# Kernel tuning notes

Measured on AMD Instinct MI355X. Metric: run time of the kernel, lower is better.

The kernel has to match this reference:

```python
import jax, jax.numpy as jnp
import numpy as np

N_NODES = 20000
N_EDGES = 320000
HID = 128
IN_NODE = 128
IN_EDGE = 128
OUT = 64
N_LAYERS = 5 - 2  # 3 layers
EPS = 1e-5


def _lin_init(k, din, dout):
    return jax.random.normal(k, (din, dout), jnp.float32) * (1.0 / np.sqrt(din))


def setup_inputs() -> dict:
    key = jax.random.key(0)
    ks = jax.random.split(key, 12)
    h = jax.random.normal(ks[0], (N_NODES, IN_NODE), jnp.float32)
    edge_index = jax.random.randint(ks[1], (2, N_EDGES), 0, N_NODES, jnp.int64)
    edge_attr = jax.random.normal(ks[2], (N_EDGES, IN_EDGE), jnp.float32)
    node_emb_W = _lin_init(ks[3], IN_NODE, HID)
    node_emb_b = jnp.zeros((HID,), jnp.float32)
    edge_emb_W = _lin_init(ks[4], IN_EDGE, HID)
    edge_emb_b = jnp.zeros((HID,), jnp.float32)
    # 5 linears (A,B,C,D,E) per layer, stacked: [L, 5, HID, HID]
    layers_W = jax.random.normal(ks[5], (N_LAYERS, 5, HID, HID), jnp.float32) * (1.0 / np.sqrt(HID))
    layers_b = jax.random.normal(ks[6], (N_LAYERS, 5, HID), jnp.float32) * 0.01
    # bn params: index 0 = node BN, index 1 = edge BN
    bn_gamma = jnp.ones((N_LAYERS, 2, HID), jnp.float32)
    bn_beta = jnp.zeros((N_LAYERS, 2, HID), jnp.float32)
    cls_W1 = _lin_init(ks[7], HID, HID)
    cls_b1 = jnp.zeros((HID,), jnp.float32)
    cls_W2 = _lin_init(ks[8], HID, OUT)
    cls_b2 = jnp.zeros((OUT,), jnp.float32)
    return dict(h=h, edge_index=edge_index, edge_attr=edge_attr,
                node_emb_W=node_emb_W, node_emb_b=node_emb_b,
                edge_emb_W=edge_emb_W, edge_emb_b=edge_emb_b,
                layers_W=layers_W, layers_b=layers_b,
                bn_gamma=bn_gamma, bn_beta=bn_beta,
                cls_W1=cls_W1, cls_b1=cls_b1, cls_W2=cls_W2, cls_b2=cls_b2)


def _bn(x, g, b):
    # BatchNorm1d in train mode: batch mean / biased variance per feature
    mu = jnp.mean(x, axis=0)
    var = jnp.mean((x - mu) ** 2, axis=0)
    return g * (x - mu) * jax.lax.rsqrt(var + EPS) + b


def _forward(h, edge_attr, edge_index, node_emb_W, node_emb_b, edge_emb_W,
             edge_emb_b, layers_W, layers_b, bn_gamma, bn_beta,
             cls_W1, cls_b1, cls_W2, cls_b2):
    n = h.shape[0]
    src, dst = edge_index[0], edge_index[1]
    h = h @ node_emb_W + node_emb_b            # [N, HID]
    e = edge_attr @ edge_emb_W + edge_emb_b    # [E, HID]
    for l in range(layers_W.shape[0]):
        W, b = layers_W[l], layers_b[l]
        Ah = h @ W[0] + b[0]
        Bh = h @ W[1] + b[1]
        Ce = e @ W[2] + b[2]
        Dh = h @ W[3] + b[3]
        Eh = h @ W[4] + b[4]
        e_hat = Ce + Dh[dst] + Eh[src]         # [E, HID]
        sigma = jax.nn.sigmoid(e_hat)
        # edge update: BN -> ReLU -> (dropout p=0) -> residual
        e = e + jax.nn.relu(_bn(e_hat, bn_gamma[l, 1], bn_beta[l, 1]))
        # node update: scatter-add of sigma * Bh[src] onto dst
        agg = jax.ops.segment_sum(sigma * Bh[src], dst, num_segments=n)
        h = h + jax.nn.relu(_bn(Ah + agg, bn_gamma[l, 0], bn_beta[l, 0]))
    out = jnp.mean(h, axis=0, keepdims=True)   # [1, HID]
    out = jax.nn.relu(out @ cls_W1 + cls_b1) @ cls_W2 + cls_b2
    return out


def reference(h, edge_index, edge_attr, node_emb_W, node_emb_b, edge_emb_W,
              edge_emb_b, layers_W, layers_b, bn_gamma, bn_beta,
              cls_W1, cls_b1, cls_W2, cls_b2):
    return _forward(h, edge_attr, edge_index, node_emb_W, node_emb_b,
                    edge_emb_W, edge_emb_b, layers_W, layers_b,
                    bn_gamma, bn_beta, cls_W1, cls_b1, cls_W2, cls_b2)
```

## Files before the change

kernel.cpp:

```cpp
#include <hip/hip_runtime.h>
#include <math.h>

#define NN 20000
#define NE 320000
#define NL 3
#define EPSV 1e-5f
#define MAXD 128
#define ASZ 2560

#define S_ESC  0
#define S_ESH  128
#define S_NSC  256
#define S_NSH  384
#define S_TOTAL 512

typedef __attribute__((ext_vector_type(8))) short bf16x8;
typedef __attribute__((ext_vector_type(4))) float f32x4;

__device__ __forceinline__ float sigf(float x) { return 1.0f / (1.0f + expf(-x)); }
__device__ __forceinline__ float b2f(unsigned short s) { return __uint_as_float((unsigned)s << 16); }
__device__ __forceinline__ unsigned short f2b(float a)
{
  unsigned u = __float_as_uint(a);
  return (unsigned short)((u + 0x7FFFu + ((u >> 16) & 1u)) >> 16);
}

__device__ __forceinline__ void bsplit(float a, unsigned short& h, unsigned short& l)
{
  unsigned u = __float_as_uint(a);
  unsigned rh = (u + 0x7FFFu + ((u >> 16) & 1u)) >> 16;
  h = (unsigned short)rh;
  float hf = __uint_as_float(rh << 16);
  float d = a - hf;
  unsigned v = __float_as_uint(d);
  l = (unsigned short)((v + 0x7FFFu + ((v >> 16) & 1u)) >> 16);
}

__global__ __launch_bounds__(256) void prep_w(const float* __restrict__ src,
                                              unsigned short* __restrict__ dh,
                                              unsigned short* __restrict__ dl, int nmat)
{
  int idx = blockIdx.x * 256 + threadIdx.x;
  if (idx >= nmat * 16384) return;
  int m = idx >> 14, r = idx & 16383, k = r >> 7, c = r & 127;
  unsigned short h, l;
  bsplit(src[idx], h, l);
  long o = ((long)m << 14) + c * 128 + k;
  dh[o] = h; dl[o] = l;
}

__device__ __forceinline__ void loadWfrags(const unsigned short* __restrict__ Wh_g,
                                           const unsigned short* __restrict__ Wl_g,
                                           int k0, int w, int r16, int g8,
                                           bf16x8& h0, bf16x8& h1, bf16x8& l0, bf16x8& l1)
{
  long o0 = (long)(w * 32 + r16) * 128 + k0 + g8 * 8;
  long o1 = o0 + 16 * 128;
  h0 = *(const bf16x8*)(Wh_g + o0);
  h1 = *(const bf16x8*)(Wh_g + o1);
  l0 = *(const bf16x8*)(Wl_g + o0);
  l1 = *(const bf16x8*)(Wl_g + o1);
}
__device__ __forceinline__ void writeA_pair(const float4& a, int row, int c4,
                                            unsigned short* Ah, unsigned short* Al)
{
  unsigned short h0, l0, h1, l1, h2, l2, h3, l3;
  bsplit(a.x, h0, l0); bsplit(a.y, h1, l1); bsplit(a.z, h2, l2); bsplit(a.w, h3, l3);
  *(uint2*)(Ah + row * 40 + c4 * 4) =
      make_uint2((unsigned)h0 | ((unsigned)h1 << 16), (unsigned)h2 | ((unsigned)h3 << 16));
  *(uint2*)(Al + row * 40 + c4 * 4) =
      make_uint2((unsigned)l0 | ((unsigned)l1 << 16), (unsigned)l2 | ((unsigned)l3 << 16));
}
__device__ __forceinline__ void writeA_bf(const float4& a, int row, int c4, unsigned short* Ah)
{
  *(uint2*)(Ah + row * 40 + c4 * 4) = make_uint2(
      (unsigned)f2b(a.x) | ((unsigned)f2b(a.y) << 16),
      (unsigned)f2b(a.z) | ((unsigned)f2b(a.w) << 16));
}

__device__ __forceinline__ void mfma_frags3r(int r16, int g8, f32x4 acc[4][2],
    const unsigned short* Ah, const unsigned short* Al,
    bf16x8 wh0, bf16x8 wh1, bf16x8 wl0, bf16x8 wl1)
{
  bf16x8 ah[4], al[4];
  #pragma unroll
  for (int rg = 0; rg < 4; ++rg) {
    ah[rg] = *(const bf16x8*)(Ah + (rg * 16 + r16) * 40 + g8 * 8);
    al[rg] = *(const bf16x8*)(Al + (rg * 16 + r16) * 40 + g8 * 8);
  }
  #pragma unroll
  for (int rg = 0; rg < 4; ++rg) {
    acc[rg][0] = __builtin_amdgcn_mfma_f32_16x16x32_bf16(ah[rg], wh0, acc[rg][0], 0, 0, 0);
    acc[rg][0] = __builtin_amdgcn_mfma_f32_16x16x32_bf16(ah[rg], wl0, acc[rg][0], 0, 0, 0);
    acc[rg][0] = __builtin_amdgcn_mfma_f32_16x16x32_bf16(al[rg], wh0, acc[rg][0], 0, 0, 0);
    acc[rg][1] = __builtin_amdgcn_mfma_f32_16x16x32_bf16(ah[rg], wh1, acc[rg][1], 0, 0, 0);
    acc[rg][1] = __builtin_amdgcn_mfma_f32_16x16x32_bf16(ah[rg], wl1, acc[rg][1], 0, 0, 0);
    acc[rg][1] = __builtin_amdgcn_mfma_f32_16x16x32_bf16(al[rg], wh1, acc[rg][1], 0, 0, 0);
  }
}

__device__ __forceinline__ void mfma_frags2r(int r16, int g8, f32x4 acc[4][2],
    const unsigned short* Ah,
    bf16x8 wh0, bf16x8 wh1, bf16x8 wl0, bf16x8 wl1)
{
  bf16x8 ah[4];
  #pragma unroll
  for (int rg = 0; rg < 4; ++rg)
    ah[rg] = *(const bf16x8*)(Ah + (rg * 16 + r16) * 40 + g8 * 8);
  #pragma unroll
  for (int rg = 0; rg < 4; ++rg) {
    acc[rg][0] = __builtin_amdgcn_mfma_f32_16x16x32_bf16(ah[rg], wh0, acc[rg][0], 0, 0, 0);
    acc[rg][0] = __builtin_amdgcn_mfma_f32_16x16x32_bf16(ah[rg], wl0, acc[rg][0], 0, 0, 0);
    acc[rg][1] = __builtin_amdgcn_mfma_f32_16x16x32_bf16(ah[rg], wh1, acc[rg][1], 0, 0, 0);
    acc[rg][1] = __builtin_amdgcn_mfma_f32_16x16x32_bf16(ah[rg], wl1, acc[rg][1], 0, 0, 0);
  }
}

#define ACC_INIT                          \
  _Pragma("unroll")                       \
  for (int rg = 0; rg < 4; ++rg)          \
    _Pragma("unroll")                     \
    for (int cg = 0; cg < 2; ++cg)        \
      acc[rg][cg] = (f32x4){0.f, 0.f, 0.f, 0.f};

__device__ __forceinline__ void mfma_core_f32(
    const float* __restrict__ A, long base, int M,
    const unsigned short* __restrict__ Wh_g, const unsigned short* __restrict__ Wl_g,
    int tid, f32x4 acc[4][2], unsigned short* Ah, unsigned short* Al)
{
  int lane = tid & 63, w = tid >> 6, r16 = lane & 15, g8 = lane >> 4;
  int r0 = tid >> 3, c4 = tid & 7;
  long g0 = base + r0, g1 = g0 + 32;
  bool v0 = g0 < M, v1 = g1 < M;
  ACC_INIT
  float4 a[4][2];
  #pragma unroll
  for (int ks = 0; ks < 4; ++ks) {
    a[ks][0] = v0 ? *(const float4*)(A + g0 * 128 + ks * 32 + c4 * 4) : make_float4(0.f, 0.f, 0.f, 0.f);
    a[ks][1] = v1 ? *(const float4*)(A + g1 * 128 + ks * 32 + c4 * 4) : make_float4(0.f, 0.f, 0.f, 0.f);
  }
  bf16x8 wc0, wc1, wc2, wc3, wn0, wn1, wn2, wn3;
  loadWfrags(Wh_g, Wl_g, 0, w, r16, g8, wc0, wc1, wc2, wc3);
  writeA_pair(a[0][0], r0, c4, Ah, Al);
  writeA_pair(a[0][1], r0 + 32, c4, Ah, Al);
  #pragma unroll
  for (int ks = 0; ks < 4; ++ks) {
    __syncthreads();
    int cb = ks & 1, nb = cb ^ 1;
    if (ks < 3) loadWfrags(Wh_g, Wl_g, 32 * (ks + 1), w, r16, g8, wn0, wn1, wn2, wn3);
    mfma_frags3r(r16, g8, acc, Ah + cb * ASZ, Al + cb * ASZ, wc0, wc1, wc2, wc3);
    if (ks < 3) {
      writeA_pair(a[ks + 1][0], r0, c4, Ah + nb * ASZ, Al + nb * ASZ);
      writeA_pair(a[ks + 1][1], r0 + 32, c4, Ah + nb * ASZ, Al + nb * ASZ);
      wc0 = wn0; wc1 = wn1; wc2 = wn2; wc3 = wn3;
    }
  }
}

__device__ __forceinline__ void mfma_core_bf16i(
    const float* __restrict__ A, const int* ridx,
    const unsigned short* __restrict__ Wh_g, const unsigned short* __restrict__ Wl_g,
    int tid, f32x4 acc[4][2], unsigned short* Ah)
{
  int lane = tid & 63, w = tid >> 6, r16 = lane & 15, g8 = lane >> 4;
  int r0 = tid >> 3, c4 = tid & 7;
  long g0 = ridx[r0], g1 = ridx[r0 + 32];
  ACC_INIT
  float4 a[4][2];
  #pragma unroll
  for (int ks = 0; ks < 4; ++ks) {
    a[ks][0] = *(const float4*)(A + g0 * 128 + ks * 32 + c4 * 4);
    a[ks][1] = *(const float4*)(A + g1 * 128 + ks * 32 + c4 * 4);
  }
  bf16x8 wc0, wc1, wc2, wc3, wn0, wn1, wn2, wn3;
  loadWfrags(Wh_g, Wl_g, 0, w, r16, g8, wc0, wc1, wc2, wc3);
  writeA_bf(a[0][0], r0, c4, Ah);
  writeA_bf(a[0][1], r0 + 32, c4, Ah);
  #pragma unroll
  for (int ks = 0; ks < 4; ++ks) {
    __syncthreads();
    int cb = ks & 1, nb = cb ^ 1;
    if (ks < 3) loadWfrags(Wh_g, Wl_g, 32 * (ks + 1), w, r16, g8, wn0, wn1, wn2, wn3);
    mfma_frags2r(r16, g8, acc, Ah + cb * ASZ, wc0, wc1, wc2, wc3);
    if (ks < 3) {
      writeA_bf(a[ks + 1][0], r0, c4, Ah + nb * ASZ);
      writeA_bf(a[ks + 1][1], r0 + 32, c4, Ah + nb * ASZ);
      wc0 = wn0; wc1 = wn1; wc2 = wn2; wc3 = wn3;
    }
  }
}

__device__ __forceinline__ void mfma_core_bf16(
    const unsigned short* __restrict__ Abf, long base,
    const unsigned short* __restrict__ Wh_g, const unsigned short* __restrict__ Wl_g,
    int tid, f32x4 acc[4][2], unsigned short* Ah)
{
  int lane = tid & 63, w = tid >> 6, r16 = lane & 15, g8 = lane >> 4;
  int row = tid >> 2, q = tid & 3;
  ACC_INIT
  long gof = (base + row) * 128 + q * 8;
  uint4 av[4];
  #pragma unroll
  for (int ks = 0; ks < 4; ++ks) av[ks] = *(const uint4*)(Abf + gof + ks * 32);
  bf16x8 wc0, wc1, wc2, wc3, wn0, wn1, wn2, wn3;
  loadWfrags(Wh_g, Wl_g, 0, w, r16, g8, wc0, wc1, wc2, wc3);
  *(uint4*)(Ah + row * 40 + q * 8) = av[0];
  #pragma unroll
  for (int ks = 0; ks < 4; ++ks) {
    __syncthreads();
    int cb = ks & 1, nb = cb ^ 1;
    if (ks < 3) loadWfrags(Wh_g, Wl_g, 32 * (ks + 1), w, r16, g8, wn0, wn1, wn2, wn3);
    mfma_frags2r(r16, g8, acc, Ah + cb * ASZ, wc0, wc1, wc2, wc3);
    if (ks < 3) {
      *(uint4*)(Ah + nb * ASZ + row * 40 + q * 8) = av[ks + 1];
      wc0 = wn0; wc1 = wn1; wc2 = wn2; wc3 = wn3;
    }
  }
}

template<bool WB>
__device__ __forceinline__ void mfma_core_upd(
    unsigned short* __restrict__ Ebf,
    const unsigned short* __restrict__ EHAT, long base,
    const unsigned short* __restrict__ Wh_g, const unsigned short* __restrict__ Wl_g,
    const float* s_sc, const float* s_sh,
    int tid, f32x4 acc[4][2], unsigned short* Ah)
{
  int lane = tid & 63, w = tid >> 6, r16 = lane & 15, g8 = lane >> 4;
  int row = tid >> 2, q = tid & 3;
  ACC_INIT
  long grow = (base + row) * 128;
  uint4 ev[4], hv[4];
  #pragma unroll
  for (int ks = 0; ks < 4; ++ks) {
    ev[ks] = *(const uint4*)(Ebf + grow + ks * 32 + q * 8);
    hv[ks] = *(const uint4*)(EHAT + grow + ks * 32 + q * 8);
  }
  bf16x8 wc0, wc1, wc2, wc3, wn0, wn1, wn2, wn3;
  loadWfrags(Wh_g, Wl_g, 0, w, r16, g8, wc0, wc1, wc2, wc3);

  #pragma unroll
  for (int ks = 0; ks < 4; ++ks) {
    int cb = ks & 1;
    int cbase = ks * 32 + q * 8;
    {
      uint4 evk = ev[ks], hvk = hv[ks];
      unsigned es[8] = {evk.x & 0xFFFFu, evk.x >> 16, evk.y & 0xFFFFu, evk.y >> 16,
                        evk.z & 0xFFFFu, evk.z >> 16, evk.w & 0xFFFFu, evk.w >> 16};
      unsigned hs[8] = {hvk.x & 0xFFFFu, hvk.x >> 16, hvk.y & 0xFFFFu, hvk.y >> 16,
                        hvk.z & 0xFFFFu, hvk.z >> 16, hvk.w & 0xFFFFu, hvk.w >> 16};
      unsigned short nv[8];
      #pragma unroll
      for (int i = 0; i < 8; ++i) {
        float v = b2f((unsigned short)es[i]) +
                  fmaxf(fmaf(s_sc[cbase + i], b2f((unsigned short)hs[i]), s_sh[cbase + i]), 0.f);
        nv[i] = f2b(v);
      }
      uint4 nq = make_uint4((unsigned)nv[0] | ((unsigned)nv[1] << 16),
                            (unsigned)nv[2] | ((unsigned)nv[3] << 16),
                            (unsigned)nv[4] | ((unsigned)nv[5] << 16),
                            (unsigned)nv[6] | ((unsigned)nv[7] << 16));
      *(uint4*)(Ah + cb * ASZ + row * 40 + q * 8) = nq;
      if (WB) *(uint4*)(Ebf + grow + cbase) = nq;
    }
    __syncthreads();
    if (ks < 3) loadWfrags(Wh_g, Wl_g, 32 * (ks + 1), w, r16, g8, wn0, wn1, wn2, wn3);
    mfma_frags2r(r16, g8, acc, Ah + cb * ASZ, wc0, wc1, wc2, wc3);
    if (ks < 3) { wc0 = wn0; wc1 = wn1; wc2 = wn2; wc3 = wn3; }
    if (ks < 2) __syncthreads();
  }
}

__device__ __forceinline__ void edge_epilogue(
    f32x4 acc[4][2], const float* __restrict__ bias,
    const int* __restrict__ srcp, const int* __restrict__ dstp,
    const float* __restrict__ Dh, const float* __restrict__ Eh,
    unsigned short* __restrict__ ehat, float* __restrict__ epart, int do_stats,
    long base, int tid)
{
  int lane = tid & 63, w = tid >> 6;
  int r16 = lane & 15, g8 = lane >> 4;
  int colA = w * 32 + r16, colB = colA + 16;
  float bA = bias[colA], bB = bias[colB];
  float s0 = 0.f, s1 = 0.f, q0 = 0.f, q1 = 0.f;
  #pragma unroll
  for (int rg = 0; rg < 4; ++rg)
    #pragma unroll
    for (int j = 0; j < 4; ++j) {
      long erow = base + rg * 16 + g8 * 4 + j;
      int si = srcp[erow], di = dstp[erow];
      const float* dhp = Dh + (long)di * 128;
      const float* ehp = Eh + (long)si * 128;
      float xA = acc[rg][0][j] + bA + dhp[colA] + ehp[colA];
      float xB = acc[rg][1][j] + bB + dhp[colB] + ehp[colB];
      ehat[erow * 128 + colA] = f2b(xA);
      ehat[erow * 128 + colB] = f2b(xB);
      s0 += xA; q0 += xA * xA; s1 += xB; q1 += xB * xB;
    }
  if (do_stats) {
    s0 += __shfl_xor(s0, 16); s0 += __shfl_xor(s0, 32);
    q0 += __shfl_xor(q0, 16); q0 += __shfl_xor(q0, 32);
    s1 += __shfl_xor(s1, 16); s1 += __shfl_xor(s1, 32);
    q1 += __shfl_xor(q1, 16); q1 += __shfl_xor(q1, 32);
    if (g8 == 0) {
      float* bp = epart + (long)blockIdx.x * 256;
      bp[colA] = s0;       bp[128 + colA] = q0;
      bp[colB] = s1;       bp[128 + colB] = q1;
    }
  }
}

__global__ __launch_bounds__(256) void gemm128(
    const float* __restrict__ A, const unsigned short* __restrict__ Wh_g,
    const unsigned short* __restrict__ Wl_g, const float* __restrict__ bias,
    float* __restrict__ C, int M)
{
  __shared__ unsigned short Ah[2 * ASZ], Al[2 * ASZ];
  int tid = threadIdx.x, lane = tid & 63, w = tid >> 6;
  int r16 = lane & 15, g8 = lane >> 4;
  long base = (long)blockIdx.x * 64;
  f32x4 acc[4][2];
  mfma_core_f32(A, base, M, Wh_g, Wl_g, tid, acc, Ah, Al);
  #pragma unroll
  for (int cg = 0; cg < 2; ++cg) {
    int col = w * 32 + cg * 16 + r16;
    float b = bias[col];
    #pragma unroll
    for (int rg = 0; rg < 4; ++rg)
      #pragma unroll
      for (int j = 0; j < 4; ++j) {
        long row = base + rg * 16 + g8 * 4 + j;
        if (row < M) C[row * 128 + col] = acc[rg][cg][j] + b;
      }
  }
}

__global__ __launch_bounds__(256) void gemm128s(
    const float* __restrict__ A, const int* __restrict__ rows,
    const unsigned short* __restrict__ Wh_g, const unsigned short* __restrict__ Wl_g,
    const float* __restrict__ bias,
    unsigned short* __restrict__ Cbf)
{
  __shared__ unsigned short Ah[2 * ASZ];
  __shared__ int ridx[64];
  int tid = threadIdx.x, lane = tid & 63, w = tid >> 6;
  int r16 = lane & 15, g8 = lane >> 4;
  long base = (long)blockIdx.x * 64;
  if (tid < 64) ridx[tid] = rows[base + tid];
  __syncthreads();
  f32x4 acc[4][2];
  mfma_core_bf16i(A, ridx, Wh_g, Wl_g, tid, acc, Ah);
  #pragma unroll
  for (int cg = 0; cg < 2; ++cg) {
    int col = w * 32 + cg * 16 + r16;
    float b = bias[col];
    #pragma unroll
    for (int rg = 0; rg < 4; ++rg)
      #pragma unroll
      for (int j = 0; j < 4; ++j) {
        long row = base + rg * 16 + g8 * 4 + j;
        Cbf[row * 128 + col] = f2b(acc[rg][cg][j] + b);
      }
  }
}

__global__ __launch_bounds__(256) void gemm128_x4(
    const float* __restrict__ A, const unsigned short* __restrict__ Wh_l,
    const unsigned short* __restrict__ Wl_l, const float* __restrict__ bl,
    float* __restrict__ o0, float* __restrict__ o1, float* __restrict__ o2,
    float* __restrict__ o3, int M)
{
  __shared__ unsigned short Ah[2 * ASZ], Al[2 * ASZ];
  int y = blockIdx.y;
  int widx = (y < 2) ? y : y + 1;
  const unsigned short* Wh_g = Wh_l + ((long)widx << 14);
  const unsigned short* Wl_g = Wl_l + ((long)widx << 14);
  const float* bias = bl + (long)widx * 128;
  float* C = (y == 0) ? o0 : (y == 1) ? o1 : (y == 2) ? o2 : o3;
  int tid = threadIdx.x, lane = tid & 63, w = tid >> 6;
  int r16 = lane & 15, g8 = lane >> 4;
  long base = (long)blockIdx.x * 64;
  f32x4 acc[4][2];
  mfma_core_f32(A, base, M, Wh_g, Wl_g, tid, acc, Ah, Al);
  #pragma unroll
  for (int cg = 0; cg < 2; ++cg) {
    int col = w * 32 + cg * 16 + r16;
    float b = bias[col];
    #pragma unroll
    for (int rg = 0; rg < 4; ++rg)
      #pragma unroll
      for (int j = 0; j < 4; ++j) {
        long row = base + rg * 16 + g8 * 4 + j;
        if (row < M) C[row * 128 + col] = acc[rg][cg][j] + b;
      }
  }
}

__global__ __launch_bounds__(256) void edge_fused0(
    const unsigned short* __restrict__ ebf,
    const unsigned short* __restrict__ Wh_g, const unsigned short* __restrict__ Wl_g,
    const float* __restrict__ bias, const int* __restrict__ srcp, const int* __restrict__ dstp,
    const float* __restrict__ Dh, const float* __restrict__ Eh,
    unsigned short* __restrict__ ehat, float* __restrict__ epart, int do_stats)
{
  __shared__ unsigned short Ah[2 * ASZ];
  int tid = threadIdx.x;
  long base = (long)blockIdx.x * 64;
  f32x4 acc[4][2];
  mfma_core_bf16(ebf, base, Wh_g, Wl_g, tid, acc, Ah);
  edge_epilogue(acc, bias, srcp, dstp, Dh, Eh, ehat, epart, do_stats, base, tid);
}

template<bool WB>
__global__ __launch_bounds__(256) void edge_fusedU(
    unsigned short* __restrict__ ebf,
    unsigned short* __restrict__ ehat,
    const float* __restrict__ scale, const float* __restrict__ shift,
    const unsigned short* __restrict__ Wh_g, const unsigned short* __restrict__ Wl_g,
    const float* __restrict__ bias, const int* __restrict__ srcp, const int* __restrict__ dstp,
    const float* __restrict__ Dh, const float* __restrict__ Eh,
    float* __restrict__ epart, int do_stats)
{
  __shared__ unsigned short Ah[2 * ASZ];
  __shared__ float s_sc[128], s_sh[128];
  int tid = threadIdx.x;
  if (tid < 128) { s_sc[tid] = scale[tid]; s_sh[tid] = shift[tid]; }
  __syncthreads();
  long base = (long)blockIdx.x * 64;
  f32x4 acc[4][2];
  mfma_core_upd<WB>(ebf, ehat, base, Wh_g, Wl_g, s_sc, s_sh, tid, acc, Ah);
  edge_epilogue(acc, bias, srcp, dstp, Dh, Eh, ehat, epart, do_stats, base, tid);
}

__global__ __launch_bounds__(256) void reduce_part(const float* __restrict__ in,
                                                   float* __restrict__ outp, int groups)
{
  int t = threadIdx.x;
  long base = (long)blockIdx.x * groups * 256;
  float acc = 0.f;
  for (int i = 0; i < groups; ++i) acc += in[base + i * 256 + t];
  outp[(long)blockIdx.x * 256 + t] = acc;
}

__global__ void finalize_bn_p(const float* __restrict__ part, int np, float invn,
                              const float* __restrict__ gamma, const float* __restrict__ beta,
                              float* __restrict__ scale, float* __restrict__ shift)
{
  int c = threadIdx.x;
  float s = 0.f, q = 0.f;
  for (int p = 0; p < np; ++p) {
    s += part[(long)p * 256 + c];
    q += part[(long)p * 256 + 128 + c];
  }
  float mu = s * invn;
  float var = q * invn - mu * mu;
  float sc = gamma[c] * rsqrtf(var + EPSV);
  scale[c] = sc;
  shift[c] = beta[c] - sc * mu;
}

__global__ __launch_bounds__(256) void hist_dst(const int* __restrict__ dst, int* __restrict__ deg)
{
  int e = blockIdx.x * 256 + threadIdx.x;
  if (e < NE) atomicAdd(&deg[dst[e]], 1);
}

__global__ __launch_bounds__(1024) void scan_deg(const int* __restrict__ deg,
                                                 int* __restrict__ rowstart, int* __restrict__ cursor)
{
  __shared__ int wsum[16];
  __shared__ int carry;
  int tid = threadIdx.x, lane = tid & 63, wid = tid >> 6;
  if (tid == 0) carry = 0;
  __syncthreads();
  for (int base = 0; base < NN; base += 1024) {
    int i = base + tid;
    int v = (i < NN) ? deg[i] : 0;
    int x = v;
    #pragma unroll
    for (int off = 1; off < 64; off <<= 1) {
      int y = __shfl_up(x, off, 64);
      if (lane >= off) x += y;
    }
    if (lane == 63) wsum[wid] = x;
    __syncthreads();
    int wpref = 0;
    for (int j = 0; j < wid; ++j) wpref += wsum[j];
    int excl = carry + wpref + x - v;
    if (i < NN) { rowstart[i] = excl; cursor[i] = excl; }
    __syncthreads();
    if (tid == 1023) carry = excl + v;
    __syncthreads();
  }
  if (tid == 0) rowstart[NN] = NE;
}

__global__ __launch_bounds__(256) void fill_csr(const int* __restrict__ dst,
                                                int* __restrict__ cursor, int* __restrict__ elist)
{
  int e = blockIdx.x * 256 + threadIdx.x;
  if (e < NE) {
    int p = atomicAdd(&cursor[dst[e]], 1);
    elist[p] = e;
  }
}

__global__ __launch_bounds__(128) void seg_sort(const int* __restrict__ rowstart,
                                                int* __restrict__ elist)
{
  __shared__ int buf[MAXD];
  __shared__ int srt[MAXD];
  int n = blockIdx.x;
  int s = rowstart[n], t = rowstart[n + 1];
  int deg = t - s;
  if (deg > MAXD) deg = MAXD;
  int tid = threadIdx.x;
  if (tid < deg) buf[tid] = elist[s + tid];
  __syncthreads();
  if (tid < deg) {
    int v = buf[tid], r = 0;
    for (int j = 0; j < deg; ++j) r += (buf[j] < v);
    srt[r] = v;
  }
  __syncthreads();
  if (tid < deg) elist[s + tid] = srt[tid];
}

__global__ __launch_bounds__(256) void perm_edges(const int* __restrict__ elist,
                                                  const int* __restrict__ src,
                                                  const int* __restrict__ dst,
                                                  int* __restrict__ srcp, int* __restrict__ dstp)
{
  int s = blockIdx.x * 256 + threadIdx.x;
  if (s < NE) {
    int e = elist[s];
    srcp[s] = src[e];
    dstp[s] = dst[e];
  }
}

__global__ __launch_bounds__(128) void gather_node(
    const unsigned short* __restrict__ ehat, const float* __restrict__ Bh,
    const int* __restrict__ srcp, const int* __restrict__ rowstart, float* __restrict__ x)
{
  __shared__ int ssrc[MAXD];
  int n = blockIdx.x;
  int s = rowstart[n], t = rowstart[n + 1];
  int deg = t - s;
  int nload = deg < MAXD ? deg : MAXD;
  int tid = threadIdx.x;
  if (tid < nload) ssrc[tid] = srcp[s + tid];
  __syncthreads();
  float acc = 0.f;
  for (int k = 0; k < nload; ++k)
    acc += sigf(b2f(ehat[(long)(s + k) * 128 + tid])) * Bh[(long)ssrc[k] * 128 + tid];
  for (int k = MAXD; k < deg; ++k)
    acc += sigf(b2f(ehat[(long)(s + k) * 128 + tid])) * Bh[(long)srcp[s + k] * 128 + tid];
  x[(long)n * 128 + tid] += acc;
}

__global__ __launch_bounds__(256) void stats128p(const float* __restrict__ x, float* __restrict__ part)
{
  __shared__ float red[8][32][8];
  int tid = threadIdx.x, tx = tid & 31, ty = tid >> 5;
  long rbase = (long)blockIdx.x * 80;
  float a0 = 0, a1 = 0, a2 = 0, a3 = 0, c0 = 0, c1 = 0, c2 = 0, c3 = 0;
  #pragma unroll
  for (int i = 0; i < 10; ++i) {
    long row = rbase + i * 8 + ty;
    float4 v = *(const float4*)(x + row * 128 + tx * 4);
    a0 += v.x; a1 += v.y; a2 += v.z; a3 += v.w;
    c0 += v.x * v.x; c1 += v.y * v.y; c2 += v.z * v.z; c3 += v.w * v.w;
  }
  red[ty][tx][0] = a0; red[ty][tx][1] = a1; red[ty][tx][2] = a2; red[ty][tx][3] = a3;
  red[ty][tx][4] = c0; red[ty][tx][5] = c1; red[ty][tx][6] = c2; red[ty][tx][7] = c3;
  __syncthreads();
  if (ty == 0) {
    float b0 = 0, b1 = 0, b2 = 0, b3 = 0, d0 = 0, d1 = 0, d2 = 0, d3 = 0;
    #pragma unroll
    for (int t = 0; t < 8; ++t) {
      b0 += red[t][tx][0]; b1 += red[t][tx][1]; b2 += red[t][tx][2]; b3 += red[t][tx][3];
      d0 += red[t][tx][4]; d1 += red[t][tx][5]; d2 += red[t][tx][6]; d3 += red[t][tx][7];
    }
    float* bp = part + (long)blockIdx.x * 256;
    bp[tx * 4 + 0] = b0; bp[tx * 4 + 1] = b1; bp[tx * 4 + 2] = b2; bp[tx * 4 + 3] = b3;
    bp[128 + tx * 4 + 0] = d0; bp[128 + tx * 4 + 1] = d1;
    bp[128 + tx * 4 + 2] = d2; bp[128 + tx * 4 + 3] = d3;
  }
}

__global__ __launch_bounds__(256) void pass2(
    float* __restrict__ dsta, const float* __restrict__ xv,
    const float* __restrict__ scale, const float* __restrict__ shift, long n4)
{
  long i = (long)blockIdx.x * 256 + threadIdx.x;
  if (i >= n4) return;
  int c = (int)(i & 31) * 4;
  float4 x = ((const float4*)xv)[i];
  float4 sc = *(const float4*)(scale + c);
  float4 sh = *(const float4*)(shift + c);
  float4 d = ((const float4*)dsta)[i];
  d.x += fmaxf(fmaf(sc.x, x.x, sh.x), 0.f);
  d.y += fmaxf(fmaf(sc.y, x.y, sh.y), 0.f);
  d.z += fmaxf(fmaf(sc.z, x.z, sh.z), 0.f);
  d.w += fmaxf(fmaf(sc.w, x.w, sh.w), 0.f);
  ((float4*)dsta)[i] = d;
}

__global__ __launch_bounds__(256) void colsum_p(const float* __restrict__ h, float* __restrict__ hpart)
{
  __shared__ float red[8][32][4];
  int tid = threadIdx.x, tx = tid & 31, ty = tid >> 5;
  long rbase = (long)blockIdx.x * 80;
  float a0 = 0, a1 = 0, a2 = 0, a3 = 0;
  #pragma unroll
  for (int i = 0; i < 10; ++i) {
    long row = rbase + i * 8 + ty;
    float4 v = *(const float4*)(h + row * 128 + tx * 4);
    a0 += v.x; a1 += v.y; a2 += v.z; a3 += v.w;
  }
  red[ty][tx][0] = a0; red[ty][tx][1] = a1; red[ty][tx][2] = a2; red[ty][tx][3] = a3;
  __syncthreads();
  if (ty == 0) {
    float b0 = 0, b1 = 0, b2 = 0, b3 = 0;
    #pragma unroll
    for (int t = 0; t < 8; ++t) {
      b0 += red[t][tx][0]; b1 += red[t][tx][1]; b2 += red[t][tx][2]; b3 += red[t][tx][3];
    }
    float* bp = hpart + (long)blockIdx.x * 128;
    bp[tx * 4 + 0] = b0; bp[tx * 4 + 1] = b1; bp[tx * 4 + 2] = b2; bp[tx * 4 + 3] = b3;
  }
}

__global__ void cls_head(const float* __restrict__ hpart,
                         const float* __restrict__ W1, const float* __restrict__ b1,
                         const float* __restrict__ W2, const float* __restrict__ b2,
                         float* __restrict__ out)
{
  __shared__ float hm[128];
  __shared__ float r1[128];
  int t = threadIdx.x;
  float s = 0.f;
  for (int p = 0; p < 250; ++p) s += hpart[(long)p * 128 + t];
  hm[t] = s * (1.0f / NN);
  __syncthreads();
  float v = b1[t];
  for (int k = 0; k < 128; ++k) v = fmaf(hm[k], W1[k * 128 + t], v);
  r1[t] = fmaxf(v, 0.f);
  __syncthreads();
  if (t < 64) {
    float o = b2[t];
    for (int k = 0; k < 128; ++k) o = fmaf(r1[k], W2[k * 64 + t], o);
    out[t] = o;
  }
}

extern "C" void kernel_launch(void* const* d_in, const int* in_sizes, int n_in,
                              void* d_out, int out_size, void* d_ws, size_t ws_size,
                              hipStream_t stream)
{
  const float* h_in  = (const float*)d_in[0];
  const int*   ei    = (const int*)d_in[1];
  const float* eattr = (const float*)d_in[2];
  const float* nW    = (const float*)d_in[3];
  const float* nb    = (const float*)d_in[4];
  const float* eW    = (const float*)d_in[5];
  const float* eb    = (const float*)d_in[6];
  const float* LW    = (const float*)d_in[7];
  const float* LB    = (const float*)d_in[8];
  const float* G     = (const float*)d_in[9];
  const float* Bt    = (const float*)d_in[10];
  const float* W1    = (const float*)d_in[11];
  const float* b1    = (const float*)d_in[12];
  const float* W2    = (const float*)d_in[13];
  const float* b2    = (const float*)d_in[14];
  float* out = (float*)d_out;

  float* ws = (float*)d_ws;
  float* f_h     = ws;
  unsigned short* f_ehat = (unsigned short*)(f_h + (long)NN * 128);
  float* f_A     = (float*)(f_ehat + (long)NE * 128);
  float* f_B     = f_A    + (long)NN * 128;
  float* f_D     = f_B    + (long)NN * 128;
  float* f_E     = f_D    + (long)NN * 128;
  float* f_stats = f_E    + (long)NN * 128;
  float* f_npart = f_stats + S_TOTAL;
  float* f_epart = f_npart + 250 * 256;
  float* f_epart2= f_epart + (long)5000 * 256;
  float* f_hpart = f_epart2 + 50 * 256;
  unsigned short* e_bf = (unsigned short*)(f_hpart + 250 * 128);
  int* i_deg      = (int*)(e_bf + (long)NE * 128);
  int* i_rowstart = i_deg + NN;
  int* i_cursor   = i_rowstart + NN + 1;
  int* i_elist    = i_cursor + NN;
  int* i_srcp     = i_elist + NE;
  int* i_dstp     = i_srcp + NE;
  size_t pw_off = ((((char*)(i_dstp + NE)) - (char*)d_ws) + 15) & ~(size_t)15;
  unsigned short* pw_h = (unsigned short*)((char*)d_ws + pw_off);
  unsigned short* pw_l = pw_h + (long)17 * 16384;
  const int* src = ei;
  const int* dst = ei + NE;

  prep_w<<<64, 256, 0, stream>>>(nW, pw_h, pw_l, 1);
  prep_w<<<64, 256, 0, stream>>>(eW, pw_h + 16384, pw_l + 16384, 1);
  prep_w<<<960, 256, 0, stream>>>(LW, pw_h + 2 * 16384, pw_l + 2 * 16384, 15);

  hipMemsetAsync(i_deg, 0, NN * sizeof(int), stream);
  hist_dst<<<(NE + 255) / 256, 256, 0, stream>>>(dst, i_deg);
  scan_deg<<<1, 1024, 0, stream>>>(i_deg, i_rowstart, i_cursor);
  fill_csr<<<(NE + 255) / 256, 256, 0, stream>>>(dst, i_cursor, i_elist);
  seg_sort<<<NN, 128, 0, stream>>>(i_rowstart, i_elist);
  perm_edges<<<(NE + 255) / 256, 256, 0, stream>>>(i_elist, src, dst, i_srcp, i_dstp);

  gemm128<<<313, 256, 0, stream>>>(h_in, pw_h, pw_l, nb, f_h, NN);
  gemm128s<<<5000, 256, 0, stream>>>(eattr, i_elist, pw_h + 16384, pw_l + 16384, eb, e_bf);

  for (int l = 0; l < NL; ++l) {
    const unsigned short* lwh = pw_h + (long)(2 + l * 5) * 16384;
    const unsigned short* lwl = pw_l + (long)(2 + l * 5) * 16384;
    const float* bl = LB + (long)l * 5 * 128;
    int last = (l == NL - 1);

    gemm128_x4<<<dim3(313, 4), 256, 0, stream>>>(f_h, lwh, lwl, bl, f_A, f_B, f_D, f_E, NN);
    if (l == 0)
      edge_fused0<<<5000, 256, 0, stream>>>(e_bf, lwh + 2 * 16384, lwl + 2 * 16384,
                                            bl + 2 * 128, i_srcp, i_dstp, f_D, f_E,
                                            f_ehat, f_epart, 1);
    else if (l == 1)
      edge_fusedU<true><<<5000, 256, 0, stream>>>(e_bf, f_ehat,
                                                  f_stats + S_ESC, f_stats + S_ESH,
                                                  lwh + 2 * 16384, lwl + 2 * 16384, bl + 2 * 128,
                                                  i_srcp, i_dstp, f_D, f_E, f_epart, 1);
    else
      edge_fusedU<false><<<5000, 256, 0, stream>>>(e_bf, f_ehat,
                                                   f_stats + S_ESC, f_stats + S_ESH,
                                                   lwh + 2 * 16384, lwl + 2 * 16384, bl + 2 * 128,
                                                   i_srcp, i_dstp, f_D, f_E, f_epart, 0);
    if (!last) {
      reduce_part<<<50, 256, 0, stream>>>(f_epart, f_epart2, 100);
      finalize_bn_p<<<1, 128, 0, stream>>>(f_epart2, 50, 1.0f / NE,
                                           G + (l * 2 + 1) * 128, Bt + (l * 2 + 1) * 128,
                                           f_stats + S_ESC, f_stats + S_ESH);
    }
    gather_node<<<NN, 128, 0, stream>>>(f_ehat, f_B, i_srcp, i_rowstart, f_A);
    stats128p<<<250, 256, 0, stream>>>(f_A, f_npart);
    finalize_bn_p<<<1, 128, 0, stream>>>(f_npart, 250, 1.0f / NN,
                                         G + (l * 2 + 0) * 128, Bt + (l * 2 + 0) * 128,
                                         f_stats + S_NSC, f_stats + S_NSH);
    pass2<<<2500, 256, 0, stream>>>(f_h, f_A, f_stats + S_NSC, f_stats + S_NSH, (long)NN * 32);
  }

  colsum_p<<<250, 256, 0, stream>>>(f_h, f_hpart);
  cls_head<<<1, 128, 0, stream>>>(f_hpart, W1, b1, W2, b2, out);
}
```

Baseline: 962.3 us.

## Fuse edge embedding GEMM with layer-0 edge GEMM, scattering via slot map

Merges the edge-embedding GEMM (previously a separate gathered kernel writing e_bf) into the layer-0 edge kernel. Edge attributes are now read contiguously in original order, the embedded edges are held in shared memory and fed straight into the C-projection MFMA, and results are scattered to their dst-sorted positions through a new slot array built in perm_edges. This removes one full write and re-read of e_bf ahead of layer 0 plus a kernel launch. In exchange, the e_bf and ehat stores become scattered, and Dh/Eh are gathered in unsorted edge order, which may hurt locality.

```diff
diff --git a/kernel.cpp b/kernel.cpp
--- a/kernel.cpp
+++ b/kernel.cpp
@@ -7,6 +7,7 @@
 #define EPSV 1e-5f
 #define MAXD 128
 #define ASZ 2560
+#define EPITCH 136
 
 #define S_ESC  0
 #define S_ESH  128
@@ -157,14 +158,14 @@
   }
 }
 
-__device__ __forceinline__ void mfma_core_bf16i(
-    const float* __restrict__ A, const int* ridx,
+__device__ __forceinline__ void mfma_core_bf16f(
+    const float* __restrict__ A, long base,
     const unsigned short* __restrict__ Wh_g, const unsigned short* __restrict__ Wl_g,
     int tid, f32x4 acc[4][2], unsigned short* Ah)
 {
   int lane = tid & 63, w = tid >> 6, r16 = lane & 15, g8 = lane >> 4;
   int r0 = tid >> 3, c4 = tid & 7;
-  long g0 = ridx[r0], g1 = ridx[r0 + 32];
+  long g0 = base + r0, g1 = g0 + 32;
   ACC_INIT
   float4 a[4][2];
   #pragma unroll
@@ -185,34 +186,6 @@
     if (ks < 3) {
       writeA_bf(a[ks + 1][0], r0, c4, Ah + nb * ASZ);
       writeA_bf(a[ks + 1][1], r0 + 32, c4, Ah + nb * ASZ);
-      wc0 = wn0; wc1 = wn1; wc2 = wn2; wc3 = wn3;
-    }
-  }
-}
-
-__device__ __forceinline__ void mfma_core_bf16(
-    const unsigned short* __restrict__ Abf, long base,
-    const unsigned short* __restrict__ Wh_g, const unsigned short* __restrict__ Wl_g,
-    int tid, f32x4 acc[4][2], unsigned short* Ah)
-{
-  int lane = tid & 63, w = tid >> 6, r16 = lane & 15, g8 = lane >> 4;
-  int row = tid >> 2, q = tid & 3;
-  ACC_INIT
-  long gof = (base + row) * 128 + q * 8;
-  uint4 av[4];
-  #pragma unroll
-  for (int ks = 0; ks < 4; ++ks) av[ks] = *(const uint4*)(Abf + gof + ks * 32);
-  bf16x8 wc0, wc1, wc2, wc3, wn0, wn1, wn2, wn3;
-  loadWfrags(Wh_g, Wl_g, 0, w, r16, g8, wc0, wc1, wc2, wc3);
-  *(uint4*)(Ah + row * 40 + q * 8) = av[0];
-  #pragma unroll
-  for (int ks = 0; ks < 4; ++ks) {
-    __syncthreads();
-    int cb = ks & 1, nb = cb ^ 1;
-    if (ks < 3) loadWfrags(Wh_g, Wl_g, 32 * (ks + 1), w, r16, g8, wn0, wn1, wn2, wn3);
-    mfma_frags2r(r16, g8, acc, Ah + cb * ASZ, wc0, wc1, wc2, wc3);
-    if (ks < 3) {
-      *(uint4*)(Ah + nb * ASZ + row * 40 + q * 8) = av[ks + 1];
       wc0 = wn0; wc1 = wn1; wc2 = wn2; wc3 = wn3;
     }
   }
@@ -335,35 +308,6 @@
   }
 }
 
-__global__ __launch_bounds__(256) void gemm128s(
-    const float* __restrict__ A, const int* __restrict__ rows,
-    const unsigned short* __restrict__ Wh_g, const unsigned short* __restrict__ Wl_g,
-    const float* __restrict__ bias,
-    unsigned short* __restrict__ Cbf)
-{
-  __shared__ unsigned short Ah[2 * ASZ];
-  __shared__ int ridx[64];
-  int tid = threadIdx.x, lane = tid & 63, w = tid >> 6;
-  int r16 = lane & 15, g8 = lane >> 4;
-  long base = (long)blockIdx.x * 64;
-  if (tid < 64) ridx[tid] = rows[base + tid];
-  __syncthreads();
-  f32x4 acc[4][2];
-  mfma_core_bf16i(A, ridx, Wh_g, Wl_g, tid, acc, Ah);
-  #pragma unroll
-  for (int cg = 0; cg < 2; ++cg) {
-    int col = w * 32 + cg * 16 + r16;
-    float b = bias[col];
-    #pragma unroll
-    for (int rg = 0; rg < 4; ++rg)
-      #pragma unroll
-      for (int j = 0; j < 4; ++j) {
-        long row = base + rg * 16 + g8 * 4 + j;
-        Cbf[row * 128 + col] = f2b(acc[rg][cg][j] + b);
-      }
-  }
-}
-
 __global__ __launch_bounds__(256) void gemm128_x4(
     const float* __restrict__ A, const unsigned short* __restrict__ Wh_l,
     const unsigned short* __restrict__ Wl_l, const float* __restrict__ bl,
@@ -396,19 +340,86 @@
   }
 }
 
-__global__ __launch_bounds__(256) void edge_fused0(
-    const unsigned short* __restrict__ ebf,
-    const unsigned short* __restrict__ Wh_g, const unsigned short* __restrict__ Wl_g,
-    const float* __restrict__ bias, const int* __restrict__ srcp, const int* __restrict__ dstp,
+__global__ __launch_bounds__(256) void edge_emb_fused0(
+    const float* __restrict__ eattr,
+    const unsigned short* __restrict__ Weh, const unsigned short* __restrict__ Wel,
+    const float* __restrict__ be,
+    const unsigned short* __restrict__ Wch, const unsigned short* __restrict__ Wcl,
+    const float* __restrict__ bc,
+    const int* __restrict__ osrc, const int* __restrict__ odst, const int* __restrict__ slot,
     const float* __restrict__ Dh, const float* __restrict__ Eh,
-    unsigned short* __restrict__ ehat, float* __restrict__ epart, int do_stats)
+    unsigned short* __restrict__ e_bf, unsigned short* __restrict__ ehat,
+    float* __restrict__ epart)
 {
   __shared__ unsigned short Ah[2 * ASZ];
-  int tid = threadIdx.x;
+  __shared__ unsigned short E0[64 * EPITCH];
+  __shared__ int sslot[64];
+  int tid = threadIdx.x, lane = tid & 63, w = tid >> 6;
+  int r16 = lane & 15, g8 = lane >> 4;
   long base = (long)blockIdx.x * 64;
+  if (tid < 64) sslot[tid] = slot[base + tid];
   f32x4 acc[4][2];
-  mfma_core_bf16(ebf, base, Wh_g, Wl_g, tid, acc, Ah);
-  edge_epilogue(acc, bias, srcp, dstp, Dh, Eh, ehat, epart, do_stats, base, tid);
+  mfma_core_bf16f(eattr, base, Weh, Wel, tid, acc, Ah);
+  #pragma unroll
+  for (int cg = 0; cg < 2; ++cg) {
+    int col = w * 32 + cg * 16 + r16;
+    float b = be[col];
+    #pragma unroll
+    for (int rg = 0; rg < 4; ++rg)
+      #pragma unroll
+      for (int j = 0; j < 4; ++j) {
+        int row = rg * 16 + g8 * 4 + j;
+        unsigned short bv = f2b(acc[rg][cg][j] + b);
+        E0[row * EPITCH + col] = bv;
+        e_bf[(long)sslot[row] * 128 + col] = bv;
+      }
+  }
+  __syncthreads();
+  ACC_INIT
+  #pragma unroll
+  for (int ks = 0; ks < 4; ++ks) {
+    bf16x8 wh0, wh1, wl0, wl1;
+    loadWfrags(Wch, Wcl, ks * 32, w, r16, g8, wh0, wh1, wl0, wl1);
+    bf16x8 ah[4];
+    #pragma unroll
+    for (int rg = 0; rg < 4; ++rg)
+      ah[rg] = *(const bf16x8*)(E0 + (rg * 16 + r16) * EPITCH + ks * 32 + g8 * 8);
+    #pragma unroll
+    for (int rg = 0; rg < 4; ++rg) {
+      acc[rg][0] = __builtin_amdgcn_mfma_f32_16x16x32_bf16(ah[rg], wh0, acc[rg][0], 0, 0, 0);
+      acc[rg][0] = __builtin_amdgcn_mfma_f32_16x16x32_bf16(ah[rg], wl0, acc[rg][0], 0, 0, 0);
+      acc[rg][1] = __builtin_amdgcn_mfma_f32_16x16x32_bf16(ah[rg], wh1, acc[rg][1], 0, 0, 0);
+      acc[rg][1] = __builtin_amdgcn_mfma_f32_16x16x32_bf16(ah[rg], wl1, acc[rg][1], 0, 0, 0);
+    }
+  }
+  int colA = w * 32 + r16, colB = colA + 16;
+  float bA = bc[colA], bB = bc[colB];
+  float s0 = 0.f, s1 = 0.f, q0 = 0.f, q1 = 0.f;
+  #pragma unroll
+  for (int rg = 0; rg < 4; ++rg)
+    #pragma unroll
+    for (int j = 0; j < 4; ++j) {
+      int row = rg * 16 + g8 * 4 + j;
+      long erow = base + row;
+      int si = osrc[erow], di = odst[erow];
+      const float* dhp = Dh + (long)di * 128;
+      const float* ehp = Eh + (long)si * 128;
+      float xA = acc[rg][0][j] + bA + dhp[colA] + ehp[colA];
+      float xB = acc[rg][1][j] + bB + dhp[colB] + ehp[colB];
+      long srow = sslot[row];
+      ehat[srow * 128 + colA] = f2b(xA);
+      ehat[srow * 128 + colB] = f2b(xB);
+      s0 += xA; q0 += xA * xA; s1 += xB; q1 += xB * xB;
+    }
+  s0 += __shfl_xor(s0, 16); s0 += __shfl_xor(s0, 32);
+  q0 += __shfl_xor(q0, 16); q0 += __shfl_xor(q0, 32);
+  s1 += __shfl_xor(s1, 16); s1 += __shfl_xor(s1, 32);
+  q1 += __shfl_xor(q1, 16); q1 += __shfl_xor(q1, 32);
+  if (g8 == 0) {
+    float* bp = epart + (long)blockIdx.x * 256;
+    bp[colA] = s0;       bp[128 + colA] = q0;
+    bp[colB] = s1;       bp[128 + colB] = q1;
+  }
 }
 
 template<bool WB>
@@ -529,13 +540,15 @@
 __global__ __launch_bounds__(256) void perm_edges(const int* __restrict__ elist,
                                                   const int* __restrict__ src,
                                                   const int* __restrict__ dst,
-                                                  int* __restrict__ srcp, int* __restrict__ dstp)
+                                                  int* __restrict__ srcp, int* __restrict__ dstp,
+                                                  int* __restrict__ slot)
 {
   int s = blockIdx.x * 256 + threadIdx.x;
   if (s < NE) {
     int e = elist[s];
     srcp[s] = src[e];
     dstp[s] = dst[e];
+    slot[e] = s;
   }
 }
 
@@ -695,7 +708,8 @@
   int* i_elist    = i_cursor + NN;
   int* i_srcp     = i_elist + NE;
   int* i_dstp     = i_srcp + NE;
-  size_t pw_off = ((((char*)(i_dstp + NE)) - (char*)d_ws) + 15) & ~(size_t)15;
+  int* i_slot     = i_dstp + NE;
+  size_t pw_off = ((((char*)(i_slot + NE)) - (char*)d_ws) + 15) & ~(size_t)15;
   unsigned short* pw_h = (unsigned short*)((char*)d_ws + pw_off);
   unsigned short* pw_l = pw_h + (long)17 * 16384;
   const int* src = ei;
@@ -710,10 +724,9 @@
   scan_deg<<<1, 1024, 0, stream>>>(i_deg, i_rowstart, i_cursor);
   fill_csr<<<(NE + 255) / 256, 256, 0, stream>>>(dst, i_cursor, i_elist);
   seg_sort<<<NN, 128, 0, stream>>>(i_rowstart, i_elist);
-  perm_edges<<<(NE + 255) / 256, 256, 0, stream>>>(i_elist, src, dst, i_srcp, i_dstp);
+  perm_edges<<<(NE + 255) / 256, 256, 0, stream>>>(i_elist, src, dst, i_srcp, i_dstp, i_slot);
 
   gemm128<<<313, 256, 0, stream>>>(h_in, pw_h, pw_l, nb, f_h, NN);
-  gemm128s<<<5000, 256, 0, stream>>>(eattr, i_elist, pw_h + 16384, pw_l + 16384, eb, e_bf);
 
   for (int l = 0; l < NL; ++l) {
     const unsigned short* lwh = pw_h + (long)(2 + l * 5) * 16384;
@@ -723,9 +736,10 @@
 
     gemm128_x4<<<dim3(313, 4), 256, 0, stream>>>(f_h, lwh, lwl, bl, f_A, f_B, f_D, f_E, NN);
     if (l == 0)
-      edge_fused0<<<5000, 256, 0, stream>>>(e_bf, lwh + 2 * 16384, lwl + 2 * 16384,
-                                            bl + 2 * 128, i_srcp, i_dstp, f_D, f_E,
-                                            f_ehat, f_epart, 1);
+      edge_emb_fused0<<<5000, 256, 0, stream>>>(eattr, pw_h + 16384, pw_l + 16384, eb,
+                                                lwh + 2 * 16384, lwl + 2 * 16384, bl + 2 * 128,
+                                                src, dst, i_slot, f_D, f_E,
+                                                e_bf, f_ehat, f_epart);
     else if (l == 1)
       edge_fusedU<true><<<5000, 256, 0, stream>>>(e_bf, f_ehat,
                                                   f_stats + S_ESC, f_stats + S_ESH,
```

Result: no change. 971.7 us (+1.0%).
